# Optimization experiments

Measured on AMD Instinct MI355X. Metric: run time of the kernel, lower is better.

## Reference

```python
import jax, jax.numpy as jnp
import numpy as np

N_NODES = 10000


def _gcn_conv(x, src, dst, W, b, n_nodes):
    # x: [N, Fin], src/dst: [E_total] (self-loops already appended)
    h = x @ W  # [N, Fout]
    ones = jnp.ones(src.shape[0], dtype=h.dtype)
    deg = jax.ops.segment_sum(ones, dst, num_segments=n_nodes)  # [N]
    dinv = jnp.where(deg > 0, jax.lax.rsqrt(deg), 0.0)
    norm = dinv[src] * dinv[dst]  # [E_total]
    msg = norm[:, None] * h[src]  # gather + scale
    out = jax.ops.segment_sum(msg, dst, num_segments=n_nodes)  # scatter-add
    return out + b


def setup_inputs() -> dict:
    key = jax.random.key(0)
    ks = jax.random.split(key, 8)
    N, Fin, H, A, E = N_NODES, 128, 256, 8, 320000
    x = jax.random.normal(ks[0], (N, Fin), dtype=jnp.float32)
    edge_index = jax.random.randint(ks[1], (2, E), 0, N, dtype=jnp.int64)
    def glorot(k, shape):
        lim = float(np.sqrt(6.0 / (shape[0] + shape[1])))
        return jax.random.uniform(k, shape, jnp.float32, -lim, lim)
    return {
        "x": x,
        "edge_index": edge_index,
        "W1": glorot(ks[2], (Fin, H)), "b1": jnp.zeros((H,), jnp.float32),
        "W2": glorot(ks[3], (H, H)), "b2": jnp.zeros((H,), jnp.float32),
        "Wh1": glorot(ks[4], (H, H)), "bh1": jnp.zeros((H,), jnp.float32),
        "Wh2": glorot(ks[5], (H, A)), "bh2": jnp.zeros((A,), jnp.float32),
    }


def reference(x, edge_index, W1, b1, W2, b2, Wh1, bh1, Wh2, bh2):
    n = x.shape[0]
    loop = jnp.arange(n, dtype=edge_index.dtype)
    src = jnp.concatenate([edge_index[0], loop])  # add self-loops
    dst = jnp.concatenate([edge_index[1], loop])
    h = jax.nn.relu(_gcn_conv(x, src, dst, W1, b1, n))
    h = jax.nn.relu(_gcn_conv(h, src, dst, W2, b2, n))
    h = jax.nn.relu(h @ Wh1 + bh1)
    q = h @ Wh2 + bh2  # [N, num_actions]
    return q
```

## Files before the change

kernel.cpp:

```cpp
#include <hip/hip_runtime.h>
#include <hip/hip_bf16.h>

typedef __hip_bfloat16 bf16;

#define FIN 128
#define HD 256
#define NA 8
#define MAXDEG 128

__device__ __forceinline__ float b2f(bf16 v) { return __bfloat162float(v); }
__device__ __forceinline__ float bfbits(unsigned u16) {
  return __uint_as_float(u16 << 16);
}
__device__ __forceinline__ unsigned short f2bfu(float f) {
  union { float f; unsigned u; } v; v.f = f;
  unsigned u = v.u;
  unsigned rb = ((u >> 16) & 1) + 0x7FFFu;
  return (unsigned short)((u + rb) >> 16);
}

struct SegOffs { int o[9]; };

__device__ __forceinline__ bool detect_f32_wave(const unsigned short* xw) {
  const uint4* p = (const uint4*)xw;
  int lane = threadIdx.x & 63;
  uint4 a = p[lane * 2], b = p[lane * 2 + 1];
  int c = 0;
  unsigned vs[8] = {a.x, a.y, a.z, a.w, b.x, b.y, b.z, b.w};
  #pragma unroll
  for (int i = 0; i < 8; ++i) {
    c += (((vs[i] >> 7) & 0xFF) >= 134);
    c += (((vs[i] >> 23) & 0xFF) >= 134);
  }
  #pragma unroll
  for (int o = 1; o < 64; o <<= 1) c += __shfl_xor(c, o);
  return c > 32;
}
__device__ __forceinline__ bool detect_i64_wave(const int* ew) {
  int lane = threadIdx.x & 63;
  int z = (ew[2 * lane + 1] == 0) ? 1 : 0;
  #pragma unroll
  for (int o = 1; o < 64; o <<= 1) z += __shfl_xor(z, o);
  return z > 32;
}

__global__ void cvt_w_kernel(const void* t0, const void* t1, const void* t2,
                             const void* t3, const void* t4, const void* t5,
                             const void* t6, const void* t7,
                             SegOffs so, float* dstf,
                             const unsigned short* xw, int* cursor, int n) {
  const bool f32w = detect_f32_wave(xw);
  int i = blockIdx.x * blockDim.x + threadIdx.x;
  if (i < n) cursor[i] = i * MAXDEG;
  if (i >= so.o[8]) return;
  const void* srcs[8] = {t0, t1, t2, t3, t4, t5, t6, t7};
  int t = 0;
  #pragma unroll
  for (int k = 1; k < 8; ++k) t += (i >= so.o[k]) ? 1 : 0;
  int off = i - so.o[t];
  const void* s = srcs[t];
  dstf[i] = f32w ? ((const float*)s)[off] : b2f(((const bf16*)s)[off]);
}

__global__ void fill_direct_kernel(const int* __restrict__ ei,
                                   unsigned* __restrict__ csr,
                                   int* __restrict__ cursor, int E) {
  const bool i64 = detect_i64_wave(ei);
  int e = blockIdx.x * blockDim.x + threadIdx.x;
  if (e >= E) return;
  int s, d;
  if (i64) { s = ei[2 * e]; d = ei[2 * (E + e)]; }
  else     { s = ei[e];     d = ei[E + e]; }
  int p = atomicAdd(&cursor[d], 1);
  csr[p] = (unsigned)s;
}

__global__ void dinv_pad_kernel(const int* __restrict__ cursor,
                                float* __restrict__ dinv,
                                unsigned* __restrict__ csr, int n) {
  int i = blockIdx.x * blockDim.x + threadIdx.x;
  if (i >= n) return;
  int e0 = i * MAXDEG;
  int cnt = cursor[i] - e0;
  dinv[i] = rsqrtf((float)cnt + 1.0f);
  int c4 = (cnt + 3) & ~3;
  for (int j = e0 + cnt; j < e0 + c4; ++j) csr[j] = 0x80000000u | (unsigned)i;
}

__global__ void agg1_kernel(const void* __restrict__ xraw,
                            const int* __restrict__ cursor,
                            const unsigned* __restrict__ csr,
                            const float* __restrict__ dinv, float* __restrict__ out,
                            int n) {
  const bool f32w = detect_f32_wave((const unsigned short*)xraw);
  int wave = (blockIdx.x * blockDim.x + threadIdx.x) >> 6;
  int lane = threadIdx.x & 63;
  if (wave >= n) return;
  const int i = wave;

  auto lr = [&](unsigned s) -> float2 {
    unsigned sr = s & 0x7FFFFFFFu;
    if (f32w) return ((const float2*)xraw)[(size_t)sr * 64 + lane];
    unsigned u = ((const unsigned*)xraw)[(size_t)sr * 32 + lane];
    return make_float2(bfbits(u & 0xFFFF), bfbits(u >> 16));
  };
  float di = dinv[i];
  auto wgt = [&](unsigned s) -> float {
    float w = dinv[s & 0x7FFFFFFFu] * di;
    return ((int)s < 0) ? 0.f : w;
  };

  float s2 = di * di;
  float2 xi = lr((unsigned)i);
  float ax = s2 * xi.x, ay = s2 * xi.y;

  int e0 = i * MAXDEG;
  int cnt = cursor[i] - e0;
  int eend = e0 + ((cnt + 3) & ~3);
  if (e0 < eend) {
    uint4 I = *(const uint4*)&csr[e0];
    float2 q0 = lr(I.x), q1 = lr(I.y), q2 = lr(I.z), q3 = lr(I.w);
    float  w0 = wgt(I.x), w1 = wgt(I.y), w2 = wgt(I.z), w3 = wgt(I.w);
    for (int e = e0 + 4; e < eend; e += 4) {
      uint4 J = *(const uint4*)&csr[e];
      float2 p0 = lr(J.x), p1 = lr(J.y), p2 = lr(J.z), p3 = lr(J.w);
      float  v0 = wgt(J.x), v1 = wgt(J.y), v2 = wgt(J.z), v3 = wgt(J.w);
      ax += w0 * q0.x; ay += w0 * q0.y;
      ax += w1 * q1.x; ay += w1 * q1.y;
      ax += w2 * q2.x; ay += w2 * q2.y;
      ax += w3 * q3.x; ay += w3 * q3.y;
      q0 = p0; q1 = p1; q2 = p2; q3 = p3;
      w0 = v0; w1 = v1; w2 = v2; w3 = v3;
    }
    ax += w0 * q0.x; ay += w0 * q0.y;
    ax += w1 * q1.x; ay += w1 * q1.y;
    ax += w2 * q2.x; ay += w2 * q2.y;
    ax += w3 * q3.x; ay += w3 * q3.y;
  }
  ((float2*)out)[(size_t)i * 64 + lane] = make_float2(ax, ay);
}

__global__ void agg2_kernel(const unsigned short* __restrict__ tmp,
                            const int* __restrict__ cursor,
                            const unsigned* __restrict__ csr,
                            const float* __restrict__ dinv, const float* __restrict__ bias,
                            float* __restrict__ out, int n) {
  int wave = (blockIdx.x * blockDim.x + threadIdx.x) >> 6;
  int lane = threadIdx.x & 63;
  if (wave >= n) return;
  const int i = wave;

  auto lr = [&](unsigned s) -> uint2 {
    return ((const uint2*)(tmp + (size_t)(s & 0x7FFFFFFFu) * 256))[lane];
  };
  float di = dinv[i];
  auto wgt = [&](unsigned s) -> float {
    float w = dinv[s & 0x7FFFFFFFu] * di;
    return ((int)s < 0) ? 0.f : w;
  };

  float s2 = di * di;
  uint2 xi = lr((unsigned)i);
  float4 b4 = ((const float4*)bias)[lane];
  float a0 = s2 * bfbits(xi.x & 0xFFFF) + b4.x;
  float a1 = s2 * bfbits(xi.x >> 16)    + b4.y;
  float a2 = s2 * bfbits(xi.y & 0xFFFF) + b4.z;
  float a3 = s2 * bfbits(xi.y >> 16)    + b4.w;

  #define CONS2(w, q) {                                            \
    a0 += w * bfbits(q.x & 0xFFFF); a1 += w * bfbits(q.x >> 16);   \
    a2 += w * bfbits(q.y & 0xFFFF); a3 += w * bfbits(q.y >> 16); }

  int e0 = i * MAXDEG;
  int cnt = cursor[i] - e0;
  int eend = e0 + ((cnt + 3) & ~3);
  if (e0 < eend) {
    uint4 I = *(const uint4*)&csr[e0];
    uint2 q0 = lr(I.x), q1 = lr(I.y), q2 = lr(I.z), q3 = lr(I.w);
    float w0 = wgt(I.x), w1 = wgt(I.y), w2 = wgt(I.z), w3 = wgt(I.w);
    for (int e = e0 + 4; e < eend; e += 4) {
      uint4 J = *(const uint4*)&csr[e];
      uint2 p0 = lr(J.x), p1 = lr(J.y), p2 = lr(J.z), p3 = lr(J.w);
      float v0 = wgt(J.x), v1 = wgt(J.y), v2 = wgt(J.z), v3 = wgt(J.w);
      CONS2(w0, q0) CONS2(w1, q1) CONS2(w2, q2) CONS2(w3, q3)
      q0 = p0; q1 = p1; q2 = p2; q3 = p3;
      w0 = v0; w1 = v1; w2 = v2; w3 = v3;
    }
    CONS2(w0, q0) CONS2(w1, q1) CONS2(w2, q2) CONS2(w3, q3)
  }
  #undef CONS2
  float4 res = make_float4(fmaxf(a0, 0.f), fmaxf(a1, 0.f), fmaxf(a2, 0.f), fmaxf(a3, 0.f));
  ((float4*)(out + (size_t)i * 256))[lane] = res;
}

template<int K, bool BIAS, bool RELU, bool FUSE_OUT, bool OUT_BF16>
__global__ __launch_bounds__(256, 3)
void gemm256(const float* __restrict__ A, const float* __restrict__ B,
             const float* __restrict__ bias, void* __restrict__ C, int N,
             const float* __restrict__ Wout, const float* __restrict__ bout,
             void* __restrict__ qout, const unsigned short* __restrict__ xw) {
  __shared__ float a_lds[16][K + 4];
  __shared__ float qsm[4][16][NA];
  const int tid = threadIdx.x;
  const int row0 = blockIdx.x * 16;

  for (int idx = tid; idx < 16 * (K / 4); idx += 256) {
    int r = idx / (K / 4);
    int k4 = idx - r * (K / 4);
    int gr = row0 + r;
    float4 v = make_float4(0.f, 0.f, 0.f, 0.f);
    if (gr < N) v = ((const float4*)A)[(size_t)gr * (K / 4) + k4];
    *reinterpret_cast<float4*>(&a_lds[r][k4 * 4]) = v;
  }
  __syncthreads();

  const int lane = tid & 63;
  const int w    = tid >> 6;
  const int cq   = lane & 15;
  const int rg   = lane >> 4;
  const int col0 = w * 64 + cq * 4;
  const int r0   = rg * 4;
  const int bcolv = w * 16 + cq;
  const float4* Bv = (const float4*)B;

  float acc[4][4] = {};
  float4 bv[4];
  #pragma unroll
  for (int p = 0; p < 4; ++p) bv[p] = Bv[p * 64 + bcolv];

  for (int k0 = 0; k0 < K; k0 += 4) {
    float4 cur[4];
    #pragma unroll
    for (int p = 0; p < 4; ++p) cur[p] = bv[p];
    if (k0 + 4 < K) {
      #pragma unroll
      for (int p = 0; p < 4; ++p) bv[p] = Bv[(k0 + 4 + p) * 64 + bcolv];
    }
    #pragma unroll
    for (int r = 0; r < 4; ++r) {
      const float4 a4 = *reinterpret_cast<const float4*>(&a_lds[r0 + r][k0]);
      acc[r][0] += a4.x * cur[0].x; acc[r][1] += a4.x * cur[0].y;
      acc[r][2] += a4.x * cur[0].z; acc[r][3] += a4.x * cur[0].w;
      acc[r][0] += a4.y * cur[1].x; acc[r][1] += a4.y * cur[1].y;
      acc[r][2] += a4.y * cur[1].z; acc[r][3] += a4.y * cur[1].w;
      acc[r][0] += a4.z * cur[2].x; acc[r][1] += a4.z * cur[2].y;
      acc[r][2] += a4.z * cur[2].z; acc[r][3] += a4.z * cur[2].w;
      acc[r][0] += a4.w * cur[3].x; acc[r][1] += a4.w * cur[3].y;
      acc[r][2] += a4.w * cur[3].z; acc[r][3] += a4.w * cur[3].w;
    }
  }

  float bb[4] = {0.f, 0.f, 0.f, 0.f};
  if (BIAS) {
    #pragma unroll
    for (int j = 0; j < 4; ++j) bb[j] = bias[col0 + j];
  }
  #pragma unroll
  for (int r = 0; r < 4; ++r) {
    #pragma unroll
    for (int j = 0; j < 4; ++j) {
      acc[r][j] += bb[j];
      if (RELU) acc[r][j] = fmaxf(acc[r][j], 0.f);
    }
  }

  if constexpr (!FUSE_OUT) {
    #pragma unroll
    for (int r = 0; r < 4; ++r) {
      int gr = row0 + r0 + r;
      if (gr < N) {
        if constexpr (OUT_BF16) {
          ushort4 pk;
          pk.x = f2bfu(acc[r][0]); pk.y = f2bfu(acc[r][1]);
          pk.z = f2bfu(acc[r][2]); pk.w = f2bfu(acc[r][3]);
          *reinterpret_cast<ushort4*>((unsigned short*)C + (size_t)gr * 256 + col0) = pk;
        } else {
          *reinterpret_cast<float4*>((float*)C + (size_t)gr * 256 + col0) =
              make_float4(acc[r][0], acc[r][1], acc[r][2], acc[r][3]);
        }
      }
    }
  } else {
    const float4* Wv = (const float4*)Wout;
    float4 w0[4], w1[4];
    #pragma unroll
    for (int i = 0; i < 4; ++i) {
      w0[i] = Wv[(size_t)(col0 + i) * 2];
      w1[i] = Wv[(size_t)(col0 + i) * 2 + 1];
    }
    float p[4][8];
    #pragma unroll
    for (int r = 0; r < 4; ++r) {
      p[r][0] = acc[r][0]*w0[0].x + acc[r][1]*w0[1].x + acc[r][2]*w0[2].x + acc[r][3]*w0[3].x;
      p[r][1] = acc[r][0]*w0[0].y + acc[r][1]*w0[1].y + acc[r][2]*w0[2].y + acc[r][3]*w0[3].y;
      p[r][2] = acc[r][0]*w0[0].z + acc[r][1]*w0[1].z + acc[r][2]*w0[2].z + acc[r][3]*w0[3].z;
      p[r][3] = acc[r][0]*w0[0].w + acc[r][1]*w0[1].w + acc[r][2]*w0[2].w + acc[r][3]*w0[3].w;
      p[r][4] = acc[r][0]*w1[0].x + acc[r][1]*w1[1].x + acc[r][2]*w1[2].x + acc[r][3]*w1[3].x;
      p[r][5] = acc[r][0]*w1[0].y + acc[r][1]*w1[1].y + acc[r][2]*w1[2].y + acc[r][3]*w1[3].y;
      p[r][6] = acc[r][0]*w1[0].z + acc[r][1]*w1[1].z + acc[r][2]*w1[2].z + acc[r][3]*w1[3].z;
      p[r][7] = acc[r][0]*w1[0].w + acc[r][1]*w1[1].w + acc[r][2]*w1[2].w + acc[r][3]*w1[3].w;
    }
    #pragma unroll
    for (int r = 0; r < 4; ++r) {
      #pragma unroll
      for (int j = 0; j < 8; ++j) {
        float s = p[r][j];
        s += __shfl_xor(s, 1); s += __shfl_xor(s, 2);
        s += __shfl_xor(s, 4); s += __shfl_xor(s, 8);
        p[r][j] = s;
      }
    }
    if (cq == 0) {
      #pragma unroll
      for (int r = 0; r < 4; ++r)
        #pragma unroll
        for (int j = 0; j < 8; ++j) qsm[w][r0 + r][j] = p[r][j];
    }
    const bool f32o = detect_f32_wave(xw);
    __syncthreads();
    if (tid < 16 * NA) {
      int row = tid >> 3, j = tid & 7;
      float v = qsm[0][row][j] + qsm[1][row][j] + qsm[2][row][j] + qsm[3][row][j]
              + bout[j];
      int gr = row0 + row;
      if (gr < N) {
        if (f32o) ((float*)qout)[(size_t)gr * NA + j] = v;
        else      ((bf16*)qout)[(size_t)gr * NA + j] = __float2bfloat16(v);
      }
    }
  }
}

extern "C" void kernel_launch(void* const* d_in, const int* in_sizes, int n_in,
                              void* d_out, int out_size, void* d_ws, size_t ws_size,
                              hipStream_t stream) {
  (void)n_in; (void)out_size; (void)ws_size;
  const void* x_raw  = d_in[0];
  const int*  ei_raw = (const int*)d_in[1];

  const int N = in_sizes[0] / FIN;
  const int E = in_sizes[1] / 2;

  SegOffs so;
  int acc = 0;
  for (int t = 0; t < 8; ++t) { so.o[t] = acc; acc += in_sizes[t + 2]; }
  so.o[8] = acc;

  char* ws = (char*)d_ws;
  size_t off = 0;
  auto walloc = [&](size_t bytes) -> void* {
    void* p = ws + off;
    off = (off + bytes + 255) & ~(size_t)255;
    return p;
  };
  float*    wf     = (float*)walloc((size_t)acc * 4);
  float*    dinv   = (float*)walloc((size_t)N * 4);
  int*      cursor = (int*)walloc((size_t)N * 4);
  unsigned* csr    = (unsigned*)walloc((size_t)N * MAXDEG * 4);
  float*    xagg   = (float*)walloc((size_t)N * FIN * 4);
  float*    bufA   = (float*)walloc((size_t)N * HD * 4);
  unsigned short* bufB16 = (unsigned short*)walloc((size_t)N * HD * 2);

  const float* w1f  = wf + so.o[0];
  const float* b1f  = wf + so.o[1];
  const float* w2f  = wf + so.o[2];
  const float* b2f  = wf + so.o[3];
  const float* wh1f = wf + so.o[4];
  const float* bh1f = wf + so.o[5];
  const float* wh2f = wf + so.o[6];
  const float* bh2f = wf + so.o[7];
  const unsigned short* xw = (const unsigned short*)x_raw;

  int cvtg = ((acc > N ? acc : N) + 255) / 256;
  cvt_w_kernel<<<cvtg, 256, 0, stream>>>(
      d_in[2], d_in[3], d_in[4], d_in[5], d_in[6], d_in[7], d_in[8], d_in[9],
      so, wf, xw, cursor, N);

  fill_direct_kernel<<<(E + 255) / 256, 256, 0, stream>>>(ei_raw, csr, cursor, E);
  dinv_pad_kernel<<<(N + 255) / 256, 256, 0, stream>>>(cursor, dinv, csr, N);

  const int ab = (N + 3) / 4;
  const int gb = (N + 15) / 16;
  agg1_kernel<<<ab, 256, 0, stream>>>(x_raw, cursor, csr, dinv, xagg, N);
  gemm256<FIN, true,  true,  false, false><<<gb, 256, 0, stream>>>(
      xagg, w1f, b1f, bufA, N, nullptr, nullptr, nullptr, xw);
  gemm256<HD,  false, false, false, true ><<<gb, 256, 0, stream>>>(
      bufA, w2f, nullptr, bufB16, N, nullptr, nullptr, nullptr, xw);
  agg2_kernel<<<ab, 256, 0, stream>>>(bufB16, cursor, csr, dinv, b2f, bufA, N);
  gemm256<HD,  true,  true,  true,  false><<<gb, 256, 0, stream>>>(
      bufA, wh1f, bh1f, nullptr, N, wh2f, bh2f, d_out, xw);
}
```

Before: 225.9 us.

## Split the two unfused GEMMs across column halves via a 2D grid

Adds a gemm_split kernel for the first two dense GEMMs. Each block computes only 128 of the 256 output columns for 16 rows, using a 2D grid with twice the blocks, 2 rows by 4 columns per thread, and launch bounds raised to 4 blocks per CU. The aim is more parallelism and occupancy with fewer registers per thread. In exchange, each A tile is loaded into LDS twice, and each thread does less arithmetic per B load. The fused head GEMM is moved into its own specialized kernel, and a macro is renamed.

```diff
diff --git a/kernel.cpp b/kernel.cpp
--- a/kernel.cpp
+++ b/kernel.cpp
@@ -167,7 +167,7 @@
   float a2 = s2 * bfbits(xi.y & 0xFFFF) + b4.z;
   float a3 = s2 * bfbits(xi.y >> 16)    + b4.w;
 
-  #define CONS2(w, q) {                                            \
+  #define C2(w, q) {                                               \
     a0 += w * bfbits(q.x & 0xFFFF); a1 += w * bfbits(q.x >> 16);   \
     a2 += w * bfbits(q.y & 0xFFFF); a3 += w * bfbits(q.y >> 16); }
 
@@ -182,23 +182,105 @@
       uint4 J = *(const uint4*)&csr[e];
       uint2 p0 = lr(J.x), p1 = lr(J.y), p2 = lr(J.z), p3 = lr(J.w);
       float v0 = wgt(J.x), v1 = wgt(J.y), v2 = wgt(J.z), v3 = wgt(J.w);
-      CONS2(w0, q0) CONS2(w1, q1) CONS2(w2, q2) CONS2(w3, q3)
+      C2(w0, q0) C2(w1, q1) C2(w2, q2) C2(w3, q3)
       q0 = p0; q1 = p1; q2 = p2; q3 = p3;
       w0 = v0; w1 = v1; w2 = v2; w3 = v3;
     }
-    CONS2(w0, q0) CONS2(w1, q1) CONS2(w2, q2) CONS2(w3, q3)
-  }
-  #undef CONS2
+    C2(w0, q0) C2(w1, q1) C2(w2, q2) C2(w3, q3)
+  }
+  #undef C2
   float4 res = make_float4(fmaxf(a0, 0.f), fmaxf(a1, 0.f), fmaxf(a2, 0.f), fmaxf(a3, 0.f));
   ((float4*)(out + (size_t)i * 256))[lane] = res;
 }
 
-template<int K, bool BIAS, bool RELU, bool FUSE_OUT, bool OUT_BF16>
+template<int K, bool BIAS, bool RELU, bool OUT_BF16>
+__global__ __launch_bounds__(256, 4)
+void gemm_split(const float* __restrict__ A, const float* __restrict__ B,
+                const float* __restrict__ bias, void* __restrict__ C, int N) {
+  __shared__ float a_lds[16][K + 4];
+  const int tid = threadIdx.x;
+  const int row0 = blockIdx.x * 16;
+  const int by   = blockIdx.y;
+
+  for (int idx = tid; idx < 16 * (K / 4); idx += 256) {
+    int r = idx / (K / 4);
+    int k4 = idx - r * (K / 4);
+    int gr = row0 + r;
+    float4 v = make_float4(0.f, 0.f, 0.f, 0.f);
+    if (gr < N) v = ((const float4*)A)[(size_t)gr * (K / 4) + k4];
+    *reinterpret_cast<float4*>(&a_lds[r][k4 * 4]) = v;
+  }
+  __syncthreads();
+
+  const int lane = tid & 63;
+  const int w    = tid >> 6;
+  const int cq   = lane & 7;
+  const int rg   = lane >> 3;
+  const int col0 = by * 128 + w * 32 + cq * 4;
+  const int r0   = rg * 2;
+  const int bcolv = by * 32 + w * 8 + cq;
+  const float4* Bv = (const float4*)B;
+
+  float acc[2][4] = {};
+  float4 bv[4];
+  #pragma unroll
+  for (int p = 0; p < 4; ++p) bv[p] = Bv[p * 64 + bcolv];
+
+  for (int k0 = 0; k0 < K; k0 += 4) {
+    float4 cur[4];
+    #pragma unroll
+    for (int p = 0; p < 4; ++p) cur[p] = bv[p];
+    if (k0 + 4 < K) {
+      #pragma unroll
+      for (int p = 0; p < 4; ++p) bv[p] = Bv[(k0 + 4 + p) * 64 + bcolv];
+    }
+    #pragma unroll
+    for (int r = 0; r < 2; ++r) {
+      const float4 a4 = *reinterpret_cast<const float4*>(&a_lds[r0 + r][k0]);
+      acc[r][0] += a4.x * cur[0].x; acc[r][1] += a4.x * cur[0].y;
+      acc[r][2] += a4.x * cur[0].z; acc[r][3] += a4.x * cur[0].w;
+      acc[r][0] += a4.y * cur[1].x; acc[r][1] += a4.y * cur[1].y;
+      acc[r][2] += a4.y * cur[1].z; acc[r][3] += a4.y * cur[1].w;
+      acc[r][0] += a4.z * cur[2].x; acc[r][1] += a4.z * cur[2].y;
+      acc[r][2] += a4.z * cur[2].z; acc[r][3] += a4.z * cur[2].w;
+      acc[r][0] += a4.w * cur[3].x; acc[r][1] += a4.w * cur[3].y;
+      acc[r][2] += a4.w * cur[3].z; acc[r][3] += a4.w * cur[3].w;
+    }
+  }
+
+  float bb[4] = {0.f, 0.f, 0.f, 0.f};
+  if (BIAS) {
+    #pragma unroll
+    for (int j = 0; j < 4; ++j) bb[j] = bias[col0 + j];
+  }
+  #pragma unroll
+  for (int r = 0; r < 2; ++r) {
+    int gr = row0 + r0 + r;
+    if (gr < N) {
+      float o0 = acc[r][0] + bb[0], o1 = acc[r][1] + bb[1];
+      float o2 = acc[r][2] + bb[2], o3 = acc[r][3] + bb[3];
+      if (RELU) {
+        o0 = fmaxf(o0, 0.f); o1 = fmaxf(o1, 0.f);
+        o2 = fmaxf(o2, 0.f); o3 = fmaxf(o3, 0.f);
+      }
+      if constexpr (OUT_BF16) {
+        ushort4 pk;
+        pk.x = f2bfu(o0); pk.y = f2bfu(o1); pk.z = f2bfu(o2); pk.w = f2bfu(o3);
+        *reinterpret_cast<ushort4*>((unsigned short*)C + (size_t)gr * 256 + col0) = pk;
+      } else {
+        *reinterpret_cast<float4*>((float*)C + (size_t)gr * 256 + col0) =
+            make_float4(o0, o1, o2, o3);
+      }
+    }
+  }
+}
+
+template<int K>
 __global__ __launch_bounds__(256, 3)
-void gemm256(const float* __restrict__ A, const float* __restrict__ B,
-             const float* __restrict__ bias, void* __restrict__ C, int N,
-             const float* __restrict__ Wout, const float* __restrict__ bout,
-             void* __restrict__ qout, const unsigned short* __restrict__ xw) {
+void gemm_fused(const float* __restrict__ A, const float* __restrict__ B,
+                const float* __restrict__ bias, int N,
+                const float* __restrict__ Wout, const float* __restrict__ bout,
+                void* __restrict__ qout, const unsigned short* __restrict__ xw) {
   __shared__ float a_lds[16][K + 4];
   __shared__ float qsm[4][16][NA];
   const int tid = threadIdx.x;
@@ -250,83 +332,60 @@
     }
   }
 
-  float bb[4] = {0.f, 0.f, 0.f, 0.f};
-  if (BIAS) {
-    #pragma unroll
-    for (int j = 0; j < 4; ++j) bb[j] = bias[col0 + j];
-  }
   #pragma unroll
   for (int r = 0; r < 4; ++r) {
     #pragma unroll
     for (int j = 0; j < 4; ++j) {
-      acc[r][j] += bb[j];
-      if (RELU) acc[r][j] = fmaxf(acc[r][j], 0.f);
-    }
-  }
-
-  if constexpr (!FUSE_OUT) {
-    #pragma unroll
-    for (int r = 0; r < 4; ++r) {
-      int gr = row0 + r0 + r;
-      if (gr < N) {
-        if constexpr (OUT_BF16) {
-          ushort4 pk;
-          pk.x = f2bfu(acc[r][0]); pk.y = f2bfu(acc[r][1]);
-          pk.z = f2bfu(acc[r][2]); pk.w = f2bfu(acc[r][3]);
-          *reinterpret_cast<ushort4*>((unsigned short*)C + (size_t)gr * 256 + col0) = pk;
-        } else {
-          *reinterpret_cast<float4*>((float*)C + (size_t)gr * 256 + col0) =
-              make_float4(acc[r][0], acc[r][1], acc[r][2], acc[r][3]);
-        }
-      }
-    }
-  } else {
-    const float4* Wv = (const float4*)Wout;
-    float4 w0[4], w1[4];
-    #pragma unroll
-    for (int i = 0; i < 4; ++i) {
-      w0[i] = Wv[(size_t)(col0 + i) * 2];
-      w1[i] = Wv[(size_t)(col0 + i) * 2 + 1];
-    }
-    float p[4][8];
-    #pragma unroll
-    for (int r = 0; r < 4; ++r) {
-      p[r][0] = acc[r][0]*w0[0].x + acc[r][1]*w0[1].x + acc[r][2]*w0[2].x + acc[r][3]*w0[3].x;
-      p[r][1] = acc[r][0]*w0[0].y + acc[r][1]*w0[1].y + acc[r][2]*w0[2].y + acc[r][3]*w0[3].y;
-      p[r][2] = acc[r][0]*w0[0].z + acc[r][1]*w0[1].z + acc[r][2]*w0[2].z + acc[r][3]*w0[3].z;
-      p[r][3] = acc[r][0]*w0[0].w + acc[r][1]*w0[1].w + acc[r][2]*w0[2].w + acc[r][3]*w0[3].w;
-      p[r][4] = acc[r][0]*w1[0].x + acc[r][1]*w1[1].x + acc[r][2]*w1[2].x + acc[r][3]*w1[3].x;
-      p[r][5] = acc[r][0]*w1[0].y + acc[r][1]*w1[1].y + acc[r][2]*w1[2].y + acc[r][3]*w1[3].y;
-      p[r][6] = acc[r][0]*w1[0].z + acc[r][1]*w1[1].z + acc[r][2]*w1[2].z + acc[r][3]*w1[3].z;
-      p[r][7] = acc[r][0]*w1[0].w + acc[r][1]*w1[1].w + acc[r][2]*w1[2].w + acc[r][3]*w1[3].w;
-    }
-    #pragma unroll
-    for (int r = 0; r < 4; ++r) {
+      acc[r][j] += bias[col0 + j];
+      acc[r][j] = fmaxf(acc[r][j], 0.f);
+    }
+  }
+
+  const float4* Wv = (const float4*)Wout;
+  float4 w0[4], w1[4];
+  #pragma unroll
+  for (int i = 0; i < 4; ++i) {
+    w0[i] = Wv[(size_t)(col0 + i) * 2];
+    w1[i] = Wv[(size_t)(col0 + i) * 2 + 1];
+  }
+  float p[4][8];
+  #pragma unroll
+  for (int r = 0; r < 4; ++r) {
+    p[r][0] = acc[r][0]*w0[0].x + acc[r][1]*w0[1].x + acc[r][2]*w0[2].x + acc[r][3]*w0[3].x;
+    p[r][1] = acc[r][0]*w0[0].y + acc[r][1]*w0[1].y + acc[r][2]*w0[2].y + acc[r][3]*w0[3].y;
+    p[r][2] = acc[r][0]*w0[0].z + acc[r][1]*w0[1].z + acc[r][2]*w0[2].z + acc[r][3]*w0[3].z;
+    p[r][3] = acc[r][0]*w0[0].w + acc[r][1]*w0[1].w + acc[r][2]*w0[2].w + acc[r][3]*w0[3].w;
+    p[r][4] = acc[r][0]*w1[0].x + acc[r][1]*w1[1].x + acc[r][2]*w1[2].x + acc[r][3]*w1[3].x;
+    p[r][5] = acc[r][0]*w1[0].y + acc[r][1]*w1[1].y + acc[r][2]*w1[2].y + acc[r][3]*w1[3].y;
+    p[r][6] = acc[r][0]*w1[0].z + acc[r][1]*w1[1].z + acc[r][2]*w1[2].z + acc[r][3]*w1[3].z;
+    p[r][7] = acc[r][0]*w1[0].w + acc[r][1]*w1[1].w + acc[r][2]*w1[2].w + acc[r][3]*w1[3].w;
+  }
+  #pragma unroll
+  for (int r = 0; r < 4; ++r) {
+    #pragma unroll
+    for (int j = 0; j < 8; ++j) {
+      float s = p[r][j];
+      s += __shfl_xor(s, 1); s += __shfl_xor(s, 2);
+      s += __shfl_xor(s, 4); s += __shfl_xor(s, 8);
+      p[r][j] = s;
+    }
+  }
+  if (cq == 0) {
+    #pragma unroll
+    for (int r = 0; r < 4; ++r)
       #pragma unroll
-      for (int j = 0; j < 8; ++j) {
-        float s = p[r][j];
-        s += __shfl_xor(s, 1); s += __shfl_xor(s, 2);
-        s += __shfl_xor(s, 4); s += __shfl_xor(s, 8);
-        p[r][j] = s;
-      }
-    }
-    if (cq == 0) {
-      #pragma unroll
-      for (int r = 0; r < 4; ++r)
-        #pragma unroll
-        for (int j = 0; j < 8; ++j) qsm[w][r0 + r][j] = p[r][j];
-    }
-    const bool f32o = detect_f32_wave(xw);
-    __syncthreads();
-    if (tid < 16 * NA) {
-      int row = tid >> 3, j = tid & 7;
-      float v = qsm[0][row][j] + qsm[1][row][j] + qsm[2][row][j] + qsm[3][row][j]
-              + bout[j];
-      int gr = row0 + row;
-      if (gr < N) {
-        if (f32o) ((float*)qout)[(size_t)gr * NA + j] = v;
-        else      ((bf16*)qout)[(size_t)gr * NA + j] = __float2bfloat16(v);
-      }
+      for (int j = 0; j < 8; ++j) qsm[w][r0 + r][j] = p[r][j];
+  }
+  const bool f32o = detect_f32_wave(xw);
+  __syncthreads();
+  if (tid < 16 * NA) {
+    int row = tid >> 3, j = tid & 7;
+    float v = qsm[0][row][j] + qsm[1][row][j] + qsm[2][row][j] + qsm[3][row][j]
+            + bout[j];
+    int gr = row0 + row;
+    if (gr < N) {
+      if (f32o) ((float*)qout)[(size_t)gr * NA + j] = v;
+      else      ((bf16*)qout)[(size_t)gr * NA + j] = __float2bfloat16(v);
     }
   }
 }
@@ -382,11 +441,11 @@
   const int ab = (N + 3) / 4;
   const int gb = (N + 15) / 16;
   agg1_kernel<<<ab, 256, 0, stream>>>(x_raw, cursor, csr, dinv, xagg, N);
-  gemm256<FIN, true,  true,  false, false><<<gb, 256, 0, stream>>>(
-      xagg, w1f, b1f, bufA, N, nullptr, nullptr, nullptr, xw);
-  gemm256<HD,  false, false, false, true ><<<gb, 256, 0, stream>>>(
-      bufA, w2f, nullptr, bufB16, N, nullptr, nullptr, nullptr, xw);
+  gemm_split<FIN, true,  true,  false><<<dim3(gb, 2), 256, 0, stream>>>(
+      xagg, w1f, b1f, bufA, N);
+  gemm_split<HD,  false, false, true ><<<dim3(gb, 2), 256, 0, stream>>>(
+      bufA, w2f, nullptr, bufB16, N);
   agg2_kernel<<<ab, 256, 0, stream>>>(bufB16, cursor, csr, dinv, b2f, bufA, N);
-  gemm256<HD,  true,  true,  true,  false><<<gb, 256, 0, stream>>>(
-      bufA, wh1f, bh1f, nullptr, N, wh2f, bh2f, d_out, xw);
-}
+  gemm_fused<HD><<<gb, 256, 0, stream>>>(
+      bufA, wh1f, bh1f, N, wh2f, bh2f, d_out, xw);
+}
```

Result: slower. 787.1 us (+248.5%).
